# Kernel tuning notes

Hardware: AMD Instinct MI355X
Metric: run time of the kernel (lower is better)

The kernel has to match this reference:

```python
import jax, jax.numpy as jnp
import numpy as np
import math

B, H, W = 2, 64, 64
D_MODEL = 192
D_STATE = 16
EXPAND = 1
D_INNER = EXPAND * D_MODEL
DT_RANK = math.ceil(D_MODEL / 16)  # 'auto' -> 12
DT_MIN, DT_MAX, DT_FLOOR = 0.001, 0.1, 0.0001


def setup_inputs() -> dict:
    key = jax.random.key(0)
    ks = jax.random.split(key, 10)
    x = jax.random.normal(ks[0], (B, H, W, D_MODEL), jnp.float32)
    in_proj_w = jax.random.normal(ks[1], (D_INNER, D_MODEL), jnp.float32) * (D_MODEL ** -0.5)
    in_proj_b = jnp.zeros((D_INNER,), jnp.float32)
    x_proj_w = jax.random.normal(ks[2], (2 * DT_RANK + 3 * D_STATE, D_INNER), jnp.float32) * (D_INNER ** -0.5)
    dt_init_std = DT_RANK ** -0.5
    dt_projT_w = jax.random.uniform(ks[3], (D_INNER, DT_RANK), jnp.float32, -dt_init_std, dt_init_std)
    dt_projL_w = jax.random.uniform(ks[4], (D_INNER, DT_RANK), jnp.float32, -dt_init_std, dt_init_std)
    # dt bias init: inverse-softplus of dt sampled log-uniform in [dt_min, dt_max]
    dt = jnp.exp(jax.random.uniform(ks[5], (D_INNER,), jnp.float32) * (math.log(DT_MAX) - math.log(DT_MIN)) + math.log(DT_MIN))
    dt = jnp.clip(dt, DT_FLOOR, None)
    inv_dt = dt + jnp.log(-jnp.expm1(-dt))
    dt_projT_b = inv_dt
    dt_projL_b = inv_dt
    A_init = jnp.tile(jnp.arange(1, D_STATE + 1, dtype=jnp.float32), (D_INNER, 1))  # [D_INNER, N]
    AT_log = jnp.log(A_init)
    AL_log = jnp.log(A_init)
    D_skip = jnp.ones((D_INNER,), jnp.float32)
    out_proj_w = jax.random.normal(ks[6], (D_MODEL, D_INNER), jnp.float32) * (D_INNER ** -0.5)
    out_proj_b = jnp.zeros((D_MODEL,), jnp.float32)
    return {"x": x, "in_proj_w": in_proj_w, "in_proj_b": in_proj_b, "x_proj_w": x_proj_w,
            "dt_projT_w": dt_projT_w, "dt_projT_b": dt_projT_b, "dt_projL_w": dt_projL_w,
            "dt_projL_b": dt_projL_b, "AT_log": AT_log, "AL_log": AL_log, "D_skip": D_skip,
            "out_proj_w": out_proj_w, "out_proj_b": out_proj_b}


def _wavefront_ssm(u, x_proj_w, dt_projT_w, dt_projT_b, dt_projL_w, dt_projL_b, AT_log, AL_log, D_skip):
    # u: [B,H,W,D_INNER]. 2D selective scan: state at (i,j) mixes top (i-1,j) and left (i,j-1).
    R, N = DT_RANK, D_STATE
    proj = jnp.einsum('bhwd,pd->bhwp', u, x_proj_w)  # [B,H,W,2R+3N]
    dtT_r = proj[..., :R]
    dtL_r = proj[..., R:2 * R]
    B_T = proj[..., 2 * R:2 * R + N]            # [B,H,W,N]
    B_L = proj[..., 2 * R + N:2 * R + 2 * N]    # [B,H,W,N]
    C = proj[..., 2 * R + 2 * N:]               # [B,H,W,N]
    deltaT = jax.nn.softplus(jnp.einsum('bhwr,dr->bhwd', dtT_r, dt_projT_w) + dt_projT_b)  # [B,H,W,D]
    deltaL = jax.nn.softplus(jnp.einsum('bhwr,dr->bhwd', dtL_r, dt_projL_w) + dt_projL_b)
    AT = -jnp.exp(AT_log)  # [D,N]
    AL = -jnp.exp(AL_log)
    dAT = jnp.exp(deltaT[..., None] * AT)  # [B,H,W,D,N]
    dAL = jnp.exp(deltaL[..., None] * AL)
    dB = (deltaT[..., None] * B_T[..., None, :] + deltaL[..., None] * B_L[..., None, :]) * u[..., None]  # [B,H,W,D,N]
    # reorder to [H,W,B,D,N] for scanning
    dAT_s = jnp.transpose(dAT, (1, 2, 0, 3, 4))
    dAL_s = jnp.transpose(dAL, (1, 2, 0, 3, 4))
    dB_s = jnp.transpose(dB, (1, 2, 0, 3, 4))

    def row_step(h_prev_row, row):  # h_prev_row: [W,B,D,N]
        dAT_r, dAL_r, dB_r = row
        top = dAT_r * h_prev_row + dB_r  # top-neighbor contribution + input, per column

        def col_step(h_left, cols):  # h_left: [B,D,N]
            t, a = cols
            h = t + a * h_left
            return h, h

        h0 = jnp.zeros_like(h_prev_row[0])
        _, h_row = jax.lax.scan(col_step, h0, (top, dAL_r))  # [W,B,D,N]
        return h_row, h_row

    h_init = jnp.zeros((W, u.shape[0], D_INNER, N), u.dtype)
    _, hs = jax.lax.scan(row_step, h_init, (dAT_s, dAL_s, dB_s))  # [H,W,B,D,N]
    h = jnp.transpose(hs, (2, 0, 1, 3, 4))  # [B,H,W,D,N]
    y = jnp.einsum('bhwdn,bhwn->bhwd', h, C) + u * D_skip
    return y


def reference(x, in_proj_w, in_proj_b, x_proj_w, dt_projT_w, dt_projT_b,
              dt_projL_w, dt_projL_b, AT_log, AL_log, D_skip, out_proj_w, out_proj_b):
    u = jax.nn.gelu(jnp.einsum('bhwc,dc->bhwd', x, in_proj_w) + in_proj_b, approximate=False)
    y = _wavefront_ssm(u, x_proj_w, dt_projT_w, dt_projT_b, dt_projL_w, dt_projL_b, AT_log, AL_log, D_skip)
    y = jax.nn.gelu(y, approximate=False)
    out = jnp.einsum('bhwd,cd->bhwc', y, out_proj_w) + out_proj_b
    return out
```

## Files before the change

kernel.cpp:

```cpp
#include <hip/hip_runtime.h>
#include <math.h>

#define DM 192
#define RNK 12
#define NS 16
#define NO2 432

#define OFF_FLAG   156672u
#define OFF_PY0    156688u
#define OFF_PY1    1729552u
#define OFF_YG     3302416u
#define OFF_DIAG   5268496u
#define OFF_TL2    6841360u
#define OFF_BC16   9987088u

typedef __attribute__((ext_vector_type(8))) short short8v;
typedef __attribute__((ext_vector_type(4))) float floatx4;

__device__ __forceinline__ float gelu_f(float x){
    return 0.5f * x * (1.0f + erff(x * 0.70710678118654752f));
}
__device__ __forceinline__ float softplus_f(float x){
    return fmaxf(x, 0.0f) + log1pf(__expf(-fabsf(x)));
}
__device__ __forceinline__ int diag_off(int s){
    return (s <= 64) ? ((s * (s + 1)) >> 1) : (2080 + (((s - 64) * (191 - s)) >> 1));
}
__device__ __forceinline__ void inv_diag(int q, int& i_out, int& j_out){
    int s;
    if (q < 2080){
        s = (int)((sqrtf(8.0f * (float)q + 1.0f) - 1.0f) * 0.5f);
        while (((s + 1) * (s + 2)) / 2 <= q) s++;
        while ((s * (s + 1)) / 2 > q) s--;
    } else {
        const int q2 = 4095 - q;
        int t = (int)((sqrtf(8.0f * (float)q2 + 1.0f) - 1.0f) * 0.5f);
        while (((t + 1) * (t + 2)) / 2 <= q2) t++;
        while ((t * (t + 1)) / 2 > q2) t--;
        s = 126 - t;
    }
    const int jmin = (s > 63) ? (s - 63) : 0;
    const int j = jmin + (q - diag_off(s));
    j_out = j;
    i_out = s - j;
}
__device__ __forceinline__ unsigned short bf16_rte(float f){
    unsigned u = __float_as_uint(f);
    unsigned r = (u + 0x7fffu + ((u >> 16) & 1u)) >> 16;
    return (unsigned short)r;
}
__device__ __forceinline__ float bf16_f(unsigned short h){
    return __uint_as_float(((unsigned)h) << 16);
}
__device__ __forceinline__ unsigned pack2bf(float lo, float hi){
    return (unsigned)bf16_rte(lo) | ((unsigned)bf16_rte(hi) << 16);
}
__device__ __forceinline__ float bl2f(unsigned v){ return __uint_as_float(v << 16); }
__device__ __forceinline__ float bh2f(unsigned v){ return __uint_as_float(v & 0xffff0000u); }
__device__ __forceinline__ void split8(float4 v0, float4 v1, short8v& hi, short8v& lo){
    float f[8] = {v0.x, v0.y, v0.z, v0.w, v1.x, v1.y, v1.z, v1.w};
    #pragma unroll
    for (int e = 0; e < 8; e++){
        unsigned short h = bf16_rte(f[e]);
        hi[e] = (short)h;
        lo[e] = (short)bf16_rte(f[e] - bf16_f(h));
    }
}

#define SW_WINH 0u
#define SW_WINL 36864u
#define SW_WCH  73728u
#define SW_WCL  156672u
#define SW_WOH  239616u
#define SW_WOL  276480u

__global__ __launch_bounds__(256) void prep_k(const float* __restrict__ Win,
                                              const float* __restrict__ xpw,
                                              const float* __restrict__ dtwT,
                                              const float* __restrict__ dtwL,
                                              const float* __restrict__ Wout,
                                              const float* __restrict__ ATl,
                                              const float* __restrict__ ALl,
                                              float* __restrict__ ws){
    unsigned short* __restrict__ wsu = (unsigned short*)ws;
    if (blockIdx.x == 612){
        __shared__ int okf;
        if (threadIdx.x == 0) okf = 1;
        __syncthreads();
        bool ok = true;
        for (int t = threadIdx.x; t < 6144; t += 256){
            const float* arr = (t < 3072) ? ATl : ALl;
            int e = (t < 3072) ? t : t - 3072;
            int n = e & 15;
            ok = ok && (fabsf(arr[e] - logf((float)(n + 1))) < 1e-5f);
        }
        if (!ok) atomicAnd(&okf, 0);
        __syncthreads();
        if (threadIdx.x == 0) ws[OFF_FLAG] = okf ? 1.0f : 0.0f;
        return;
    }
    int idx = blockIdx.x * 256 + threadIdx.x;
    float w;
    unsigned hioff, looff, rel;
    if (idx < 36864){
        w = Win[idx]; hioff = SW_WINH; looff = SW_WINL; rel = idx;
    } else if (idx < 119808){
        int t = idx - 36864;
        int o = t / DM, c = t - o * DM;
        float acc = 0.f;
        if (o < 192){
            #pragma unroll
            for (int r = 0; r < RNK; r++) acc += dtwT[o * RNK + r] * xpw[r * DM + c];
        } else if (o < 384){
            int d2 = o - 192;
            #pragma unroll
            for (int r = 0; r < RNK; r++) acc += dtwL[d2 * RNK + r] * xpw[(RNK + r) * DM + c];
        } else {
            acc = xpw[(2 * RNK + (o - 384)) * DM + c];
        }
        w = acc; hioff = SW_WCH; looff = SW_WCL; rel = t;
    } else if (idx < 156672){
        int t = idx - 119808;
        w = Wout[t]; hioff = SW_WOH; looff = SW_WOL; rel = t;
    } else return;
    unsigned short h = bf16_rte(w);
    wsu[hioff + rel] = h;
    wsu[looff + rel] = bf16_rte(w - bf16_f(h));
}

__global__ __launch_bounds__(256) void proj_k(const float* __restrict__ x,
                                              const float* __restrict__ inb,
                                              const float* __restrict__ dtTb,
                                              const float* __restrict__ dtLb,
                                              float* __restrict__ ws){
    __shared__ float u_t[16][196];
    __shared__ float g2[16][436];
    const unsigned short* __restrict__ wsu = (const unsigned short*)ws;
    const int bx = blockIdx.x;
    const int b = bx >> 8;
    const int Q0 = (bx & 255) * 16;
    const int tid = threadIdx.x;
    const int wv = tid >> 6, lane = tid & 63;
    const int lr = lane & 15, lg = lane >> 4;

    int ic, jc;
    inv_diag(Q0 + lr, ic, jc);
    const size_t xrow = ((size_t)(b << 12) + (size_t)(ic * 64 + jc)) * 192;

    short8v xh[6], xl[6];
    #pragma unroll
    for (int ks = 0; ks < 6; ks++){
        const float* xp = x + xrow + ks * 32 + lg * 8;
        split8(*(const float4*)xp, *(const float4*)(xp + 4), xh[ks], xl[ks]);
    }
    {
        floatx4 ac0 = {0.f,0.f,0.f,0.f}, ac1 = {0.f,0.f,0.f,0.f}, ac2 = {0.f,0.f,0.f,0.f};
        const int n0 = wv * 48;
        #pragma unroll
        for (int ks = 0; ks < 6; ks++){
            const size_t rb = (size_t)(n0 + lr) * 192 + ks * 32 + lg * 8;
            const short8v bh0 = *(const short8v*)(wsu + SW_WINH + rb);
            const short8v bl0 = *(const short8v*)(wsu + SW_WINL + rb);
            const short8v bh1 = *(const short8v*)(wsu + SW_WINH + rb + 16*192);
            const short8v bl1 = *(const short8v*)(wsu + SW_WINL + rb + 16*192);
            const short8v bh2 = *(const short8v*)(wsu + SW_WINH + rb + 32*192);
            const short8v bl2 = *(const short8v*)(wsu + SW_WINL + rb + 32*192);
            ac0 = __builtin_amdgcn_mfma_f32_16x16x32_bf16(xh[ks], bh0, ac0, 0, 0, 0);
            ac1 = __builtin_amdgcn_mfma_f32_16x16x32_bf16(xh[ks], bh1, ac1, 0, 0, 0);
            ac2 = __builtin_amdgcn_mfma_f32_16x16x32_bf16(xh[ks], bh2, ac2, 0, 0, 0);
            ac0 = __builtin_amdgcn_mfma_f32_16x16x32_bf16(xh[ks], bl0, ac0, 0, 0, 0);
            ac1 = __builtin_amdgcn_mfma_f32_16x16x32_bf16(xh[ks], bl1, ac1, 0, 0, 0);
            ac2 = __builtin_amdgcn_mfma_f32_16x16x32_bf16(xh[ks], bl2, ac2, 0, 0, 0);
            ac0 = __builtin_amdgcn_mfma_f32_16x16x32_bf16(xl[ks], bh0, ac0, 0, 0, 0);
            ac1 = __builtin_amdgcn_mfma_f32_16x16x32_bf16(xl[ks], bh1, ac1, 0, 0, 0);
            ac2 = __builtin_amdgcn_mfma_f32_16x16x32_bf16(xl[ks], bh2, ac2, 0, 0, 0);
        }
        const float b0 = inb[n0 + lr], b1 = inb[n0 + 16 + lr], b2 = inb[n0 + 32 + lr];
        #pragma unroll
        for (int r = 0; r < 4; r++){
            const int pl = lg * 4 + r;
            u_t[pl][n0 + lr]      = gelu_f(ac0[r] + b0);
            u_t[pl][n0 + 16 + lr] = gelu_f(ac1[r] + b1);
            u_t[pl][n0 + 32 + lr] = gelu_f(ac2[r] + b2);
        }
    }
    __syncthreads();

    {
        float* __restrict__ u_dg = ws + OFF_DIAG;
        #pragma unroll
        for (int pass = 0; pass < 3; pass++){
            const int plane = pass * 64 + (tid >> 2);
            const int posq = (tid & 3) * 4;
            float4 v = make_float4(u_t[posq + 0][plane], u_t[posq + 1][plane],
                                   u_t[posq + 2][plane], u_t[posq + 3][plane]);
            *(float4*)&u_dg[(size_t)(b * 192 + plane) * 4096 + Q0 + posq] = v;
        }
    }

    short8v uh[6], ul[6];
    #pragma unroll
    for (int ks = 0; ks < 6; ks++){
        const float* up = &u_t[lr][ks * 32 + lg * 8];
        split8(*(const float4*)up, *(const float4*)(up + 4), uh[ks], ul[ks]);
    }
    const int t0 = wv * 7;
    const int cnt = (wv == 3) ? 6 : 7;
    for (int tp = 0; tp < cnt; tp += 2){
        const bool dual = (tp + 1 < cnt);
        const int n0a = (t0 + tp) * 16, n0b = dual ? (t0 + tp + 1) * 16 : n0a;
        floatx4 acA = {0.f,0.f,0.f,0.f}, acB = {0.f,0.f,0.f,0.f};
        #pragma unroll
        for (int ks = 0; ks < 6; ks++){
            const size_t ra = (size_t)(n0a + lr) * 192 + ks * 32 + lg * 8;
            const short8v bhA = *(const short8v*)(wsu + SW_WCH + ra);
            const short8v blA = *(const short8v*)(wsu + SW_WCL + ra);
            acA = __builtin_amdgcn_mfma_f32_16x16x32_bf16(uh[ks], bhA, acA, 0, 0, 0);
            acA = __builtin_amdgcn_mfma_f32_16x16x32_bf16(uh[ks], blA, acA, 0, 0, 0);
            acA = __builtin_amdgcn_mfma_f32_16x16x32_bf16(ul[ks], bhA, acA, 0, 0, 0);
            if (dual){
                const size_t rbb = (size_t)(n0b + lr) * 192 + ks * 32 + lg * 8;
                const short8v bhB = *(const short8v*)(wsu + SW_WCH + rbb);
                const short8v blB = *(const short8v*)(wsu + SW_WCL + rbb);
                acB = __builtin_amdgcn_mfma_f32_16x16x32_bf16(uh[ks], bhB, acB, 0, 0, 0);
                acB = __builtin_amdgcn_mfma_f32_16x16x32_bf16(uh[ks], blB, acB, 0, 0, 0);
                acB = __builtin_amdgcn_mfma_f32_16x16x32_bf16(ul[ks], bhB, acB, 0, 0, 0);
            }
        }
        #pragma unroll
        for (int half = 0; half < 2; half++){
            if (half == 1 && !dual) break;
            const floatx4 ac = half ? acB : acA;
            const int o = (half ? n0b : n0a) + lr;
            float bb = 0.f; int mode = 2;
            if (o < 192){ bb = dtTb[o]; mode = 0; }
            else if (o < 384){ bb = dtLb[o - 192]; mode = 1; }
            #pragma unroll
            for (int r = 0; r < 4; r++){
                float v = ac[r];
                if (mode < 2) v = softplus_f(v + bb);
                g2[lg * 4 + r][o] = v;
            }
        }
    }
    __syncthreads();

    {
        float* __restrict__ tl_dg = ws + OFF_TL2;
        const int plane = tid >> 2;
        const int posq = (tid & 3) * 4;
        #pragma unroll
        for (int pass = 0; pass < 3; pass++){
            const int o = pass * 64 + plane;
            float4 w0 = make_float4(g2[posq + 0][o], g2[posq + 0][192 + o],
                                    g2[posq + 1][o], g2[posq + 1][192 + o]);
            float4 w1 = make_float4(g2[posq + 2][o], g2[posq + 2][192 + o],
                                    g2[posq + 3][o], g2[posq + 3][192 + o]);
            float* base = &tl_dg[(size_t)(b * 192 + o) * 8192 + (size_t)(Q0 + posq) * 2];
            *(float4*)&base[0] = w0;
            *(float4*)&base[4] = w1;
        }
        if (tid < 192){
            const int pl = tid >> 4;
            const int pos = tid & 15;
            const float s0 = g2[pos][384 + pl * 4 + 0];
            const float s1 = g2[pos][384 + pl * 4 + 1];
            const float s2 = g2[pos][384 + pl * 4 + 2];
            const float s3 = g2[pos][384 + pl * 4 + 3];
            uint2 v = make_uint2(pack2bf(s0, s1), pack2bf(s2, s3));
            uint2* dst = (uint2*)(ws + OFF_BC16) + (size_t)(b * 12 + pl) * 4096 + Q0 + pos;
            *dst = v;
        }
    }
}

#define LOADSET(pfx, sv) do {                                                   \
    const int sc_ = (sv) < 126 ? (sv) : 126;                                    \
    const int jmin_ = (sc_ > 63) ? (sc_ - 63) : 0;                              \
    pfx##_q = diag_off(sc_) - jmin_ + j;                                        \
    pfx##_u = pu[pfx##_q];                                                      \
    pfx##_tv = ptl[pfx##_q];                                                    \
    pfx##_bt = pBT[pfx##_q]; pfx##_bl = pBL[pfx##_q]; pfx##_cc = pC[pfx##_q];   \
} while (0)

#define STEP(pfx, sv) do {                                                      \
    const float dT_ = pfx##_tv.x, dL_ = pfx##_tv.y, u_ = pfx##_u;               \
    const float bt_[4] = {bl2f(pfx##_bt.x), bh2f(pfx##_bt.x),                   \
                          bl2f(pfx##_bt.y), bh2f(pfx##_bt.y)};                  \
    const float bl_[4] = {bl2f(pfx##_bl.x), bh2f(pfx##_bl.x),                   \
                          bl2f(pfx##_bl.y), bh2f(pfx##_bl.y)};                  \
    const float cc_[4] = {bl2f(pfx##_cc.x), bh2f(pfx##_cc.x),                   \
                          bl2f(pfx##_cc.y), bh2f(pfx##_cc.y)};                  \
    const int q_ = pfx##_q;                                                     \
    LOADSET(pfx, (sv) + 6);                                                     \
    float da_[4], dl_[4];                                                       \
    if (sflag){                                                                 \
        const float E_ = __expf(-dT_), F_ = __expf(-dL_);                       \
        da_[0] = __expf(nA1 * dT_); dl_[0] = __expf(nA1 * dL_);                 \
        da_[1] = da_[0] * E_; da_[2] = da_[1] * E_; da_[3] = da_[2] * E_;       \
        dl_[1] = dl_[0] * F_; dl_[2] = dl_[1] * F_; dl_[3] = dl_[2] * F_;       \
    } else {                                                                    \
        da_[0] = __expf(dT_ * ATr[0]); da_[1] = __expf(dT_ * ATr[1]);           \
        da_[2] = __expf(dT_ * ATr[2]); da_[3] = __expf(dT_ * ATr[3]);           \
        dl_[0] = __expf(dL_ * ALr[0]); dl_[1] = __expf(dL_ * ALr[1]);           \
        dl_[2] = __expf(dL_ * ALr[2]); dl_[3] = __expf(dL_ * ALr[3]);           \
    }                                                                           \
    const int ic_ = (sv) - j;                                                   \
    const bool act_ = ((unsigned)ic_) < 64u;                                    \
    const float udT_ = u_ * dT_, udL_ = u_ * dL_;                               \
    float y_ = 0.f;                                                             \
    _Pragma("unroll")                                                           \
    for (int k = 0; k < 4; k++){                                                \
        float hl_ = __shfl_up(h[k], 1u, 64);                                    \
        hl_ = (j == 0) ? 0.f : hl_;                                             \
        float hn_ = fmaf(da_[k], h[k], fmaf(dl_[k], hl_, fmaf(udT_, bt_[k], udL_ * bl_[k]))); \
        h[k] = act_ ? hn_ : h[k];                                               \
        y_ = fmaf(hn_, cc_[k], y_);                                             \
    }                                                                           \
    if (act_) ylds[wv][q_] = y_;                                                \
} while (0)

__global__ __launch_bounds__(128, 2) void scan_k(const float* __restrict__ ATl,
                                                 const float* __restrict__ ALl,
                                                 float* __restrict__ ws){
    __shared__ float ylds[2][4096];
    const int bx = blockIdx.x;
    const int half = (bx >= 384) ? 1 : 0;
    const int bd = bx - half * 384;
    const int b = bd / 192, d = bd - b * 192;
    const int tid = threadIdx.x;
    const int wv = tid >> 6, j = tid & 63;
    const int n0 = half * 8 + wv * 4;
    const int ng = half * 2 + wv;

    const float* __restrict__ pu = ws + OFF_DIAG + (size_t)bd * 4096;
    const float2* __restrict__ ptl = (const float2*)(ws + OFF_TL2 + (size_t)bd * 8192);
    const uint2* __restrict__ bc16 = (const uint2*)(ws + OFF_BC16) + (size_t)(b * 12) * 4096;
    const uint2* __restrict__ pBT = bc16 + (size_t)(0 + ng) * 4096;
    const uint2* __restrict__ pBL = bc16 + (size_t)(4 + ng) * 4096;
    const uint2* __restrict__ pC  = bc16 + (size_t)(8 + ng) * 4096;
    float* __restrict__ pY = ws + (half ? OFF_PY1 : OFF_PY0) + (size_t)bd * 4096;

    const bool sflag = (ws[OFF_FLAG] > 0.5f);
    const float nA1 = -(float)(n0 + 1);
    float ATr[4], ALr[4];
    if (!sflag){
        #pragma unroll
        for (int k = 0; k < 4; k++){
            ATr[k] = -expf(ATl[d * NS + n0 + k]);
            ALr[k] = -expf(ALl[d * NS + n0 + k]);
        }
    } else {
        #pragma unroll
        for (int k = 0; k < 4; k++){ ATr[k] = 0.f; ALr[k] = 0.f; }
    }
    float h[4] = {0.f, 0.f, 0.f, 0.f};

    int a_q, b_q, c_q, d_q, e_q, f_q;
    float a_u; float2 a_tv; uint2 a_bt, a_bl, a_cc;
    float b_u; float2 b_tv; uint2 b_bt, b_bl, b_cc;
    float c_u; float2 c_tv; uint2 c_bt, c_bl, c_cc;
    float d_u; float2 d_tv; uint2 d_bt, d_bl, d_cc;
    float e_u; float2 e_tv; uint2 e_bt, e_bl, e_cc;
    float f_u; float2 f_tv; uint2 f_bt, f_bl, f_cc;
    LOADSET(a, 0);
    LOADSET(b, 1);
    LOADSET(c, 2);
    LOADSET(d, 3);
    LOADSET(e, 4);
    LOADSET(f, 5);

    for (int s = 0; s < 132; s += 6){
        STEP(a, s);
        STEP(b, s + 1);
        STEP(c, s + 2);
        STEP(d, s + 3);
        STEP(e, s + 4);
        STEP(f, s + 5);
    }

    __syncthreads();
    for (int idx = tid; idx < 4096; idx += 128)
        pY[idx] = ylds[0][idx] + ylds[1][idx];
}

__global__ __launch_bounds__(256) void ysum_k(const float* __restrict__ Dskp,
                                              float* __restrict__ ws){
    __shared__ float yl[4096];
    const int bd = blockIdx.x;
    const int d = bd % 192;
    const int tid = threadIdx.x;
    const float* __restrict__ p0 = ws + OFF_PY0 + (size_t)bd * 4096;
    const float* __restrict__ p1 = ws + OFF_PY1 + (size_t)bd * 4096;
    const float* __restrict__ pu = ws + OFF_DIAG + (size_t)bd * 4096;
    float* __restrict__ yg = ws + OFF_YG + (size_t)bd * 4096;
    const float Dsk = Dskp[d];
    #pragma unroll
    for (int k = 0; k < 16; k++){
        const int idx = tid + k * 256;
        yl[idx] = gelu_f(p0[idx] + p1[idx] + pu[idx] * Dsk);
    }
    __syncthreads();
    #pragma unroll
    for (int k = 0; k < 16; k++){
        const int idx = tid + k * 256;
        const int i = idx >> 6, jj = idx & 63;
        const int s = i + jj;
        const int jmin = (s > 63) ? (s - 63) : 0;
        yg[idx] = yl[diag_off(s) + jj - jmin];
    }
}

__global__ __launch_bounds__(256) void out_k(const float* __restrict__ Wob,
                                             float* __restrict__ ws,
                                             float* __restrict__ out){
    __shared__ float yg_t[16][196];
    const unsigned short* __restrict__ wsu = (const unsigned short*)ws;
    const int P0 = blockIdx.x * 16;
    const int b = P0 >> 12;
    const int prel = P0 & 4095;
    const int tid = threadIdx.x;

    {
        const float* __restrict__ ygp = ws + OFF_YG;
        #pragma unroll
        for (int pass = 0; pass < 3; pass++){
            const int plane = pass * 64 + (tid >> 2);
            const int posq = (tid & 3) * 4;
            float4 v = *(const float4*)&ygp[(size_t)(b * 192 + plane) * 4096 + prel + posq];
            yg_t[posq + 0][plane] = v.x;
            yg_t[posq + 1][plane] = v.y;
            yg_t[posq + 2][plane] = v.z;
            yg_t[posq + 3][plane] = v.w;
        }
    }
    __syncthreads();

    const int wv = tid >> 6, lane = tid & 63;
    const int lr = lane & 15, lg = lane >> 4;

    short8v yh[6], yl2[6];
    #pragma unroll
    for (int ks = 0; ks < 6; ks++){
        const float* yp = &yg_t[lr][ks * 32 + lg * 8];
        split8(*(const float4*)yp, *(const float4*)(yp + 4), yh[ks], yl2[ks]);
    }
    {
        floatx4 ac0 = {0.f,0.f,0.f,0.f}, ac1 = {0.f,0.f,0.f,0.f}, ac2 = {0.f,0.f,0.f,0.f};
        const int n0 = wv * 48;
        #pragma unroll
        for (int ks = 0; ks < 6; ks++){
            const size_t rb = (size_t)(n0 + lr) * 192 + ks * 32 + lg * 8;
            const short8v bh0 = *(const short8v*)(wsu + SW_WOH + rb);
            const short8v bl0 = *(const short8v*)(wsu + SW_WOL + rb);
            const short8v bh1 = *(const short8v*)(wsu + SW_WOH + rb + 16*192);
            const short8v bl1 = *(const short8v*)(wsu + SW_WOL + rb + 16*192);
            const short8v bh2 = *(const short8v*)(wsu + SW_WOH + rb + 32*192);
            const short8v bl2 = *(const short8v*)(wsu + SW_WOL + rb + 32*192);
            ac0 = __builtin_amdgcn_mfma_f32_16x16x32_bf16(yh[ks], bh0, ac0, 0, 0, 0);
            ac1 = __builtin_amdgcn_mfma_f32_16x16x32_bf16(yh[ks], bh1, ac1, 0, 0, 0);
            ac2 = __builtin_amdgcn_mfma_f32_16x16x32_bf16(yh[ks], bh2, ac2, 0, 0, 0);
            ac0 = __builtin_amdgcn_mfma_f32_16x16x32_bf16(yh[ks], bl0, ac0, 0, 0, 0);
            ac1 = __builtin_amdgcn_mfma_f32_16x16x32_bf16(yh[ks], bl1, ac1, 0, 0, 0);
            ac2 = __builtin_amdgcn_mfma_f32_16x16x32_bf16(yh[ks], bl2, ac2, 0, 0, 0);
            ac0 = __builtin_amdgcn_mfma_f32_16x16x32_bf16(yl2[ks], bh0, ac0, 0, 0, 0);
            ac1 = __builtin_amdgcn_mfma_f32_16x16x32_bf16(yl2[ks], bh1, ac1, 0, 0, 0);
            ac2 = __builtin_amdgcn_mfma_f32_16x16x32_bf16(yl2[ks], bh2, ac2, 0, 0, 0);
        }
        const float b0 = Wob[n0 + lr], b1 = Wob[n0 + 16 + lr], b2 = Wob[n0 + 32 + lr];
        #pragma unroll
        for (int r = 0; r < 4; r++){
            const int pos = P0 + lg * 4 + r;
            out[(size_t)pos * 192 + n0 + lr]      = ac0[r] + b0;
            out[(size_t)pos * 192 + n0 + 16 + lr] = ac1[r] + b1;
            out[(size_t)pos * 192 + n0 + 32 + lr] = ac2[r] + b2;
        }
    }
}

extern "C" void kernel_launch(void* const* d_in, const int* in_sizes, int n_in,
                              void* d_out, int out_size, void* d_ws, size_t ws_size,
                              hipStream_t stream) {
    const float* x    = (const float*)d_in[0];
    const float* Win  = (const float*)d_in[1];
    const float* Winb = (const float*)d_in[2];
    const float* xpw  = (const float*)d_in[3];
    const float* dtTw = (const float*)d_in[4];
    const float* dtTb = (const float*)d_in[5];
    const float* dtLw = (const float*)d_in[6];
    const float* dtLb = (const float*)d_in[7];
    const float* ATl  = (const float*)d_in[8];
    const float* ALl  = (const float*)d_in[9];
    const float* Dsk  = (const float*)d_in[10];
    const float* Wo   = (const float*)d_in[11];
    const float* Wob  = (const float*)d_in[12];
    float* out = (float*)d_out;
    float* ws  = (float*)d_ws;

    hipLaunchKernelGGL(prep_k,   dim3(613), dim3(256), 0, stream, Win, xpw, dtTw, dtLw, Wo, ATl, ALl, ws);
    hipLaunchKernelGGL(proj_k,   dim3(512), dim3(256), 0, stream, x, Winb, dtTb, dtLb, ws);
    hipLaunchKernelGGL(scan_k,   dim3(768), dim3(128), 0, stream, ATl, ALl, ws);
    hipLaunchKernelGGL(ysum_k,   dim3(384), dim3(256), 0, stream, Dsk, ws);
    hipLaunchKernelGGL(out_k,    dim3(512), dim3(256), 0, stream, Wob, ws, out);
}
```

Measured before the change: 124.3 us.

## Stage u and dt diagonals in LDS, accumulate scan output via global atomics

```diff
diff --git a/kernel.cpp b/kernel.cpp
--- a/kernel.cpp
+++ b/kernel.cpp
@@ -278,8 +278,8 @@
     const int sc_ = (sv) < 126 ? (sv) : 126;                                    \
     const int jmin_ = (sc_ > 63) ? (sc_ - 63) : 0;                              \
     pfx##_q = diag_off(sc_) - jmin_ + j;                                        \
-    pfx##_u = pu[pfx##_q];                                                      \
-    pfx##_tv = ptl[pfx##_q];                                                    \
+    pfx##_u = utl[pfx##_q];                                                     \
+    pfx##_tv = *(const float2*)&utl[4096 + 2 * pfx##_q];                        \
     pfx##_bt = pBT[pfx##_q]; pfx##_bl = pBL[pfx##_q]; pfx##_cc = pC[pfx##_q];   \
 } while (0)
 
@@ -292,7 +292,7 @@
     const float cc_[4] = {bl2f(pfx##_cc.x), bh2f(pfx##_cc.x),                   \
                           bl2f(pfx##_cc.y), bh2f(pfx##_cc.y)};                  \
     const int q_ = pfx##_q;                                                     \
-    LOADSET(pfx, (sv) + 6);                                                     \
+    LOADSET(pfx, (sv) + 3);                                                     \
     float da_[4], dl_[4];                                                       \
     if (sflag){                                                                 \
         const float E_ = __expf(-dT_), F_ = __expf(-dL_);                       \
@@ -317,13 +317,13 @@
         h[k] = act_ ? hn_ : h[k];                                               \
         y_ = fmaf(hn_, cc_[k], y_);                                             \
     }                                                                           \
-    if (act_) ylds[wv][q_] = y_;                                                \
+    if (act_) atomicAdd(&pY[q_], y_);                                           \
 } while (0)
 
-__global__ __launch_bounds__(128, 2) void scan_k(const float* __restrict__ ATl,
-                                                 const float* __restrict__ ALl,
-                                                 float* __restrict__ ws){
-    __shared__ float ylds[2][4096];
+__global__ __launch_bounds__(128) void scan_k(const float* __restrict__ ATl,
+                                              const float* __restrict__ ALl,
+                                              float* __restrict__ ws){
+    __shared__ float utl[12288];
     const int bx = blockIdx.x;
     const int half = (bx >= 384) ? 1 : 0;
     const int bd = bx - half * 384;
@@ -333,13 +333,23 @@
     const int n0 = half * 8 + wv * 4;
     const int ng = half * 2 + wv;
 
-    const float* __restrict__ pu = ws + OFF_DIAG + (size_t)bd * 4096;
-    const float2* __restrict__ ptl = (const float2*)(ws + OFF_TL2 + (size_t)bd * 8192);
+    {
+        const float4* su = (const float4*)(ws + OFF_DIAG + (size_t)bd * 4096);
+        float4* du = (float4*)utl;
+        #pragma unroll
+        for (int k = 0; k < 8; k++) du[tid + k * 128] = su[tid + k * 128];
+        const float4* st = (const float4*)(ws + OFF_TL2 + (size_t)bd * 8192);
+        float4* dt = (float4*)(utl + 4096);
+        #pragma unroll
+        for (int k = 0; k < 16; k++) dt[tid + k * 128] = st[tid + k * 128];
+    }
+    __syncthreads();
+
     const uint2* __restrict__ bc16 = (const uint2*)(ws + OFF_BC16) + (size_t)(b * 12) * 4096;
     const uint2* __restrict__ pBT = bc16 + (size_t)(0 + ng) * 4096;
     const uint2* __restrict__ pBL = bc16 + (size_t)(4 + ng) * 4096;
     const uint2* __restrict__ pC  = bc16 + (size_t)(8 + ng) * 4096;
-    float* __restrict__ pY = ws + (half ? OFF_PY1 : OFF_PY0) + (size_t)bd * 4096;
+    float* __restrict__ pY = ws + (wv ? OFF_PY1 : OFF_PY0) + (size_t)bd * 4096;
 
     const bool sflag = (ws[OFF_FLAG] > 0.5f);
     const float nA1 = -(float)(n0 + 1);
@@ -356,32 +366,19 @@
     }
     float h[4] = {0.f, 0.f, 0.f, 0.f};
 
-    int a_q, b_q, c_q, d_q, e_q, f_q;
+    int a_q, b_q, c_q;
     float a_u; float2 a_tv; uint2 a_bt, a_bl, a_cc;
     float b_u; float2 b_tv; uint2 b_bt, b_bl, b_cc;
     float c_u; float2 c_tv; uint2 c_bt, c_bl, c_cc;
-    float d_u; float2 d_tv; uint2 d_bt, d_bl, d_cc;
-    float e_u; float2 e_tv; uint2 e_bt, e_bl, e_cc;
-    float f_u; float2 f_tv; uint2 f_bt, f_bl, f_cc;
     LOADSET(a, 0);
     LOADSET(b, 1);
     LOADSET(c, 2);
-    LOADSET(d, 3);
-    LOADSET(e, 4);
-    LOADSET(f, 5);
-
-    for (int s = 0; s < 132; s += 6){
+
+    for (int s = 0; s < 129; s += 3){
         STEP(a, s);
         STEP(b, s + 1);
         STEP(c, s + 2);
-        STEP(d, s + 3);
-        STEP(e, s + 4);
-        STEP(f, s + 5);
-    }
-
-    __syncthreads();
-    for (int idx = tid; idx < 4096; idx += 128)
-        pY[idx] = ylds[0][idx] + ylds[1][idx];
+    }
 }
 
 __global__ __launch_bounds__(256) void ysum_k(const float* __restrict__ Dskp,
@@ -499,6 +496,7 @@
 
     hipLaunchKernelGGL(prep_k,   dim3(613), dim3(256), 0, stream, Win, xpw, dtTw, dtLw, Wo, ATl, ALl, ws);
     hipLaunchKernelGGL(proj_k,   dim3(512), dim3(256), 0, stream, x, Winb, dtTb, dtLb, ws);
+    hipMemsetAsync(ws + OFF_PY0, 0, (size_t)2 * 384 * 4096 * sizeof(float), stream);
     hipLaunchKernelGGL(scan_k,   dim3(768), dim3(128), 0, stream, ATl, ALl, ws);
     hipLaunchKernelGGL(ysum_k,   dim3(384), dim3(256), 0, stream, Dsk, ws);
     hipLaunchKernelGGL(out_k,    dim3(512), dim3(256), 0, stream, Wob, ws, out);
```

After: 137.9 us. 1.11x slower.
